# Performance work log

Hardware: AMD Instinct MI355X
Metric: run time of the kernel (lower is better)

The kernel has to match this reference:

```python
import jax, jax.numpy as jnp
import numpy as np

D = 1024          # d_model
DQ = D // 4       # embedding dim (d_model//4)
DH = D // 2       # head hidden (d_model//2)
P = 6             # n_digit_positions = max_int_digits + n_decimal_digits
NOPS, NPT = 9, 10
B, T = 8, 2048


def _ln(x, g, b, eps=1e-5):
    m = jnp.mean(x, axis=-1, keepdims=True)
    v = jnp.mean(jnp.square(x - m), axis=-1, keepdims=True)
    return (x - m) * jax.lax.rsqrt(v + eps) * g + b


def _xavier(key, shape):
    fan_in, fan_out = shape[-2], shape[-1]
    lim = np.sqrt(6.0 / (fan_in + fan_out))
    return jax.random.uniform(key, shape, jnp.float32, -lim, lim)


def setup_inputs() -> dict:
    key = jax.random.key(0)
    ks = jax.random.split(key, 20)
    inp = {
        'hidden': jax.random.normal(ks[0], (B, T, D), jnp.float32),
        'operation_type': jax.random.randint(ks[1], (B,), 0, NOPS),
        'param_type': jax.random.randint(ks[2], (B, T), 0, NPT),
        # embeddings (std=0.02 like the torch init)
        'op_embed': 0.02 * jax.random.normal(ks[3], (NOPS, DQ), jnp.float32),
        'pt_embed': 0.02 * jax.random.normal(ks[4], (NPT, DQ), jnp.float32),
        'pos_embed': 0.02 * jax.random.normal(ks[5], (P, DQ), jnp.float32),
        # context_proj: Linear(D + D//2 -> D) + LayerNorm(D)
        'ctx_w': _xavier(ks[6], (D + D // 2, D)),
        'ctx_b': jnp.zeros((D,), jnp.float32),
        'ctx_g': jnp.ones((D,), jnp.float32),
        'ctx_beta': jnp.zeros((D,), jnp.float32),
        # sign_head: Linear(D->DH), LN(DH), Linear(DH->3)
        'sign_w1': _xavier(ks[7], (D, DH)),
        'sign_b1': jnp.zeros((DH,), jnp.float32),
        'sign_g': jnp.ones((DH,), jnp.float32),
        'sign_beta': jnp.zeros((DH,), jnp.float32),
        'sign_w2': _xavier(ks[8], (DH, 3)),
        'sign_b2': jnp.zeros((3,), jnp.float32),
        # digit heads stacked over positions: Linear(D+DQ->DH), LN(DH), Linear(DH->10)
        'dig_w1': _xavier(ks[9], (P, D + DQ, DH)),
        'dig_b1': jnp.zeros((P, DH), jnp.float32),
        'dig_g': jnp.ones((P, DH), jnp.float32),
        'dig_beta': jnp.zeros((P, DH), jnp.float32),
        'dig_w2': _xavier(ks[10], (P, DH, 10)),
        'dig_b2': jnp.zeros((P, 10), jnp.float32),
        'aux_w1': _xavier(ks[11], (D, DH)),
        'aux_b1': jnp.zeros((DH,), jnp.float32),
        'aux_w2': _xavier(ks[12], (DH, 1)),
        'aux_b2': jnp.zeros((1,), jnp.float32),
    }
    return inp


def reference(hidden, operation_type, param_type, op_embed, pt_embed, pos_embed,
              ctx_w, ctx_b, ctx_g, ctx_beta,
              sign_w1, sign_b1, sign_g, sign_beta, sign_w2, sign_b2,
              dig_w1, dig_b1, dig_g, dig_beta, dig_w2, dig_b2,
              aux_w1, aux_b1, aux_w2, aux_b2):
    b, t, d = hidden.shape
    gelu = lambda x: jax.nn.gelu(x, approximate=False)  # torch nn.GELU default

    op_emb = jnp.broadcast_to(op_embed[operation_type][:, None, :], (b, t, DQ))
    pm_emb = pt_embed[param_type]                       # [B,T,DQ]
    ctx_in = jnp.concatenate([hidden, op_emb, pm_emb], axis=-1)  # [B,T,1.5D]
    context = gelu(_ln(ctx_in @ ctx_w + ctx_b, ctx_g, ctx_beta))  # [B,T,D]

    sh = gelu(_ln(context @ sign_w1 + sign_b1, sign_g, sign_beta))
    sign_logits = sh @ sign_w2 + sign_b2                # [B,T,3]

    # digit heads, vectorized over position. concat(context, pos_emb[p]) @ W1
    # == context @ W1[:, :D] + pos_emb[p] @ W1[:, D:]
    h = (jnp.einsum('btd,pdh->btph', context, dig_w1[:, :D, :])
         + jnp.einsum('pq,pqh->ph', pos_embed, dig_w1[:, D:, :])
         + dig_b1)                                      # [B,T,P,DH]
    h = gelu(_ln(h, dig_g, dig_beta))
    digit_logits = jnp.einsum('btph,pho->btpo', h, dig_w2) + dig_b2  # [B,T,P,10]

    aux_value = gelu(context @ aux_w1 + aux_b1) @ aux_w2 + aux_b2    # [B,T,1]

    return sign_logits, digit_logits, aux_value
```

## Files before the change

### kernel.cpp

```cpp
#include <hip/hip_runtime.h>
#include <hip/hip_bf16.h>

typedef unsigned short u16;
typedef __attribute__((ext_vector_type(8))) __bf16 bf16x8;
typedef __attribute__((ext_vector_type(4))) float f32x4;

typedef __attribute__((address_space(1))) const void GVoid;
typedef __attribute__((address_space(3))) void LVoid;

__device__ __forceinline__ void async_load16(const u16* g, u16* l) {
    __builtin_amdgcn_global_load_lds((GVoid*)g, (LVoid*)l, 16, 0, 0);
}

__device__ __forceinline__ float bf2f(u16 u) {
    union { unsigned i; float f; } v; v.i = ((unsigned)u) << 16; return v.f;
}
__device__ __forceinline__ u16 f2bf(float f) {
    union { float f; unsigned i; } v; v.f = f;
    unsigned r = (v.i + 0x7FFFu + ((v.i >> 16) & 1u)) >> 16;
    return (u16)r;
}
__device__ __forceinline__ float gelu_f(float x) {
    float t = x * fmaf(0.0356774081f, x * x, 0.7978845608f);
    float e = __expf(2.0f * t);
    float r = 1.0f / (e + 1.0f);
    return x - x * r;
}

#define OP_E   0
#define PT_E   2304
#define POS_E  4864
#define CTX_B  6400
#define CTX_G  7424
#define CTX_BE 8448
#define S_B1   9472
#define S_G    9984
#define S_BE   10496
#define S_B2   11008
#define D_G    11012
#define D_BE   14084
#define D_B2   17156
#define A_B1   17216
#define A_B2   17728

struct SmallTab {
    const float* src[15];
    int off[15];
    int cnt[15];
};

__global__ __launch_bounds__(256) void convert_small(SmallTab tab, u16* __restrict__ dst)
{
    int idx = blockIdx.x * 256 + threadIdx.x;
#pragma unroll
    for (int e = 0; e < 15; ++e) {
        if (idx < tab.cnt[e]) {
            dst[tab.off[e] + idx] = f2bf(tab.src[e][idx]);
            return;
        }
        idx -= tab.cnt[e];
    }
}

__global__ __launch_bounds__(256) void transpose_all(
    const float* __restrict__ ctx_w, const float* __restrict__ sign_w1,
    const float* __restrict__ aux_w1, const float* __restrict__ dig_w1,
    u16* __restrict__ ctxWt, u16* __restrict__ BtAll)
{
    __shared__ u16 tl[32][33];
    int z = blockIdx.z;
    const float* src; u16* dst; size_t srcOff = 0; int srcLd, cols;
    if (z == 8) { src = ctx_w; dst = ctxWt; srcLd = 1024; cols = 1024; }
    else {
        srcLd = 512; cols = 512;
        if (z == 0) src = sign_w1;
        else if (z == 1) src = aux_w1;
        else { src = dig_w1; srcOff = (size_t)(z - 2) * 1280 * 512; }
        dst = BtAll + (size_t)z * 512 * 1024;
    }
    int n0 = blockIdx.x * 32;
    if (n0 >= cols) return;
    int k0 = blockIdx.y * 32;
    int t = threadIdx.x;
    int r = t >> 3;
    int c4 = (t & 7) * 4;
    float4 v = *(const float4*)&src[srcOff + (size_t)(k0 + r) * srcLd + n0 + c4];
    tl[r][c4 + 0] = f2bf(v.x); tl[r][c4 + 1] = f2bf(v.y);
    tl[r][c4 + 2] = f2bf(v.z); tl[r][c4 + 3] = f2bf(v.w);
    __syncthreads();
    ushort4 o;
    o.x = tl[c4 + 0][r]; o.y = tl[c4 + 1][r]; o.z = tl[c4 + 2][r]; o.w = tl[c4 + 3][r];
    *(ushort4*)&dst[(size_t)(n0 + r) * 1024 + k0 + c4] = o;
}

__global__ __launch_bounds__(256) void precompute_bias(
    const float* __restrict__ ctx_w, const float* __restrict__ dig_w1,
    const float* __restrict__ op_embed, const float* __restrict__ pt_embed,
    const float* __restrict__ pos_embed, const float* __restrict__ dig_b1,
    const int* __restrict__ op_type,
    float* __restrict__ E_op, float* __restrict__ P_pt, float* __restrict__ dbias)
{
    int idx = blockIdx.x * 256 + threadIdx.x;
    if (idx < 8192) {
        int b = idx >> 10, n = idx & 1023;
        const float* e = op_embed + op_type[b] * 256;
        float s = 0.f;
        for (int q = 0; q < 256; ++q)
            s += e[q] * ctx_w[(size_t)(1024 + q) * 1024 + n];
        E_op[idx] = s;
    } else if (idx < 18432) {
        int i = idx - 8192;
        int v = i >> 10, n = i & 1023;
        const float* e = pt_embed + v * 256;
        float s = 0.f;
        for (int q = 0; q < 256; ++q)
            s += e[q] * ctx_w[(size_t)(1280 + q) * 1024 + n];
        P_pt[i] = s;
    } else if (idx < 21504) {
        int i = idx - 18432;
        int p = i >> 9, h = i & 511;
        const float* e = pos_embed + p * 256;
        float s = dig_b1[p * 512 + h];
        for (int q = 0; q < 256; ++q)
            s += e[q] * dig_w1[(size_t)p * 1280 * 512 + (size_t)(1024 + q) * 512 + h];
        dbias[i] = s;
    }
}

__global__ __launch_bounds__(256) void build_vec(
    const u16* __restrict__ csm, const float* __restrict__ dbias,
    float* __restrict__ biasAll, float* __restrict__ gammaAll,
    float* __restrict__ betaAll)
{
    int n = blockIdx.x * 256 + threadIdx.x;
    float bi, g, be;
    if (n < 512) {
        bi = bf2f(csm[S_B1 + n]); g = bf2f(csm[S_G + n]); be = bf2f(csm[S_BE + n]);
    } else if (n < 1024) {
        bi = bf2f(csm[A_B1 + n - 512]); g = 1.f; be = 0.f;
    } else {
        int h = n - 1024;
        bi = dbias[h]; g = bf2f(csm[D_G + h]); be = bf2f(csm[D_BE + h]);
    }
    biasAll[n] = bi; gammaAll[n] = g; betaAll[n] = be;
}

__global__ __launch_bounds__(256) void build_w2pad(
    const float* __restrict__ sign_w2, const float* __restrict__ dig_w2,
    const float* __restrict__ aux_w2, u16* __restrict__ W2pad)
{
    int idx = blockIdx.x * 256 + threadIdx.x;
    int row = idx >> 12, k = idx & 4095;
    int r = row >> 4, o = row & 15;
    float v = 0.f;
    if (r == 0) {
        if (o < 3 && k < 512) v = sign_w2[k * 3 + o];
    } else if (r == 7) {
        if (o == 0 && k >= 512 && k < 1024) v = aux_w2[k - 512];
    } else {
        int p = r - 1, lo = 1024 + p * 512;
        if (o < 10 && k >= lo && k < lo + 512) v = dig_w2[(size_t)p * 5120 + (k - lo) * 10 + o];
    }
    W2pad[idx] = f2bf(v);
}

__global__ __launch_bounds__(512) void gemm_head_8ph(
    const u16* __restrict__ A, const u16* __restrict__ Bt, u16* __restrict__ C,
    int M)
{
    __shared__ u16 smem[65536];
    const int tid = threadIdx.x;
    const int wid = tid >> 6, lane = tid & 63;
    const int quad = lane >> 4, r16 = lane & 15;
    const int wm = wid >> 2, wn = wid & 3;

    const int Mtiles = M >> 8;
    int flat = blockIdx.x + blockIdx.y * gridDim.x;
    int cpx = (Mtiles * 16) >> 3;
    int swz = (flat & 7) * cpx + (flat >> 3);
    int bm = swz % Mtiles, bn = swz / Mtiles;
    const int m0 = bm << 8, n0 = bn << 8;

    const int rb = tid >> 3;
    const int cx = ((tid & 7) ^ (rb & 7)) * 8;
    const u16* gA = A + (size_t)(m0 + rb) * 1024 + cx;
    const u16* gB = Bt + (size_t)(n0 + rb) * 1024 + cx;

#define STAGE(arr, h, tt) do { \
        u16* _d = smem + ((((tt) & 1) * 2 + (arr)) * 2 + (h)) * 8192 + wid * 512; \
        const u16* _s = ((arr) ? gB : gA) + (size_t)((h) * 128) * 1024 + (tt) * 64; \
        async_load16(_s, _d); \
        async_load16(_s + (size_t)64 * 1024, _d + 4096); \
    } while (0)

    STAGE(0, 0, 0); STAGE(0, 1, 0); STAGE(1, 0, 0); STAGE(1, 1, 0);
    STAGE(0, 0, 1); STAGE(0, 1, 1); STAGE(1, 0, 1);
    asm volatile("s_waitcnt vmcnt(6)" ::: "memory");
    asm volatile("s_barrier" ::: "memory");

    f32x4 acc[8][4] = {};
    const int kx0 = ((quad) ^ (r16 & 7)) * 8;
    const int kx1 = ((4 + quad) ^ (r16 & 7)) * 8;

#define QUAD(MF0, NF0) \
        _Pragma("unroll") \
        for (int ks = 0; ks < 2; ++ks) \
            _Pragma("unroll") \
            for (int mi = 0; mi < 4; ++mi) \
                _Pragma("unroll") \
                for (int nj = 0; nj < 2; ++nj) \
                    acc[(MF0) + mi][(NF0) + nj] = \
                        __builtin_amdgcn_mfma_f32_16x16x32_bf16( \
                            afr[(MF0) + mi][ks], bfr[(NF0) + nj][ks], \
                            acc[(MF0) + mi][(NF0) + nj], 0, 0, 0);

    for (int t = 0; t < 16; ++t) {
        const int cur = t & 1;
        const u16* sA = smem + cur * 32768 + wm * 8192 + r16 * 64;
        const u16* sB = smem + cur * 32768 + 16384 + (wn >> 1) * 8192
                        + ((wn & 1) * 64 + r16) * 64;

        if (t + 1 < 16) STAGE(1, 1, t + 1);
        bf16x8 afr[8][2], bfr[4][2];
#pragma unroll
        for (int mf = 0; mf < 8; ++mf) {
            afr[mf][0] = *(const bf16x8*)&sA[mf * 1024 + kx0];
            afr[mf][1] = *(const bf16x8*)&sA[mf * 1024 + kx1];
        }
#pragma unroll
        for (int nf = 0; nf < 4; ++nf) {
            bfr[nf][0] = *(const bf16x8*)&sB[nf * 1024 + kx0];
            bfr[nf][1] = *(const bf16x8*)&sB[nf * 1024 + kx1];
        }
        __builtin_amdgcn_s_setprio(1);
        QUAD(0, 0)
        __builtin_amdgcn_s_setprio(0);
        asm volatile("s_waitcnt lgkmcnt(0)" ::: "memory");
        __builtin_amdgcn_sched_barrier(0);
        asm volatile("s_barrier" ::: "memory");
        __builtin_amdgcn_sched_barrier(0);

        if (t + 2 < 16) STAGE(0, 0, t + 2);
        __builtin_amdgcn_sched_barrier(0);
        __builtin_amdgcn_s_setprio(1);
        QUAD(0, 2)
        __builtin_amdgcn_s_setprio(0);
        __builtin_amdgcn_sched_barrier(0);
        asm volatile("s_barrier" ::: "memory");
        __builtin_amdgcn_sched_barrier(0);

        if (t + 2 < 16) STAGE(0, 1, t + 2);
        __builtin_amdgcn_sched_barrier(0);
        __builtin_amdgcn_s_setprio(1);
        QUAD(4, 0)
        __builtin_amdgcn_s_setprio(0);
        __builtin_amdgcn_sched_barrier(0);
        asm volatile("s_barrier" ::: "memory");
        __builtin_amdgcn_sched_barrier(0);

        if (t + 2 < 16) STAGE(1, 0, t + 2);
        __builtin_amdgcn_sched_barrier(0);
        __builtin_amdgcn_s_setprio(1);
        QUAD(4, 2)
        __builtin_amdgcn_s_setprio(0);
        __builtin_amdgcn_sched_barrier(0);
        if (t < 14)       asm volatile("s_waitcnt vmcnt(6)" ::: "memory");
        else if (t == 14) asm volatile("s_waitcnt vmcnt(0)" ::: "memory");
        asm volatile("s_barrier" ::: "memory");
    }
#undef QUAD
#undef STAGE

#pragma unroll
    for (int mf = 0; mf < 8; ++mf) {
#pragma unroll
        for (int nf = 0; nf < 4; ++nf) {
            size_t base = (size_t)(m0 + wm * 128 + mf * 16 + quad * 4) * 4096
                          + n0 + wn * 64 + nf * 16 + r16;
#pragma unroll
            for (int r = 0; r < 4; ++r)
                C[base + (size_t)r * 4096] = f2bf(acc[mf][nf][r]);
        }
    }
}

__global__ __launch_bounds__(256) void gemm_f32a(
    const float* __restrict__ A, const u16* __restrict__ Bt, u16* __restrict__ C,
    int M, int N, int K)
{
    __shared__ u16 As[128 * 32];
    __shared__ u16 Bs[128 * 32];
    const int tid = threadIdx.x;
    const int wid = tid >> 6, lane = tid & 63;
    const int m0 = blockIdx.x * 128, n0 = blockIdx.y * 128;
    const int mw = (wid >> 1) * 64, nw = (wid & 1) * 64;
    const int quad = lane >> 4, r16 = lane & 15;

    f32x4 acc[4][4] = {};

    const int srow = wid * 32 + (lane >> 2);
    const int scol = (lane & 3) * 8;
    const u16* gB = Bt + (size_t)(n0 + srow) * K + scol;
    u16* lB = Bs + wid * 32 * 32;

    const int r0 = tid >> 2;
    const int c8 = (tid & 3) * 8;

    for (int k0 = 0; k0 < K; k0 += 32) {
        async_load16(gB + k0, lB);
        async_load16(gB + k0 + (size_t)16 * K, lB + 16 * 32);
        const float* p0 = &A[(size_t)(m0 + r0) * K + k0 + c8];
        const float* p1 = &A[(size_t)(m0 + 64 + r0) * K + k0 + c8];
        float4 x = *(const float4*)p0, y = *(const float4*)(p0 + 4);
        float4 u = *(const float4*)p1, w = *(const float4*)(p1 + 4);
        uint4 a0, a1;
        a0.x = f2bf(x.x) | ((unsigned)f2bf(x.y) << 16);
        a0.y = f2bf(x.z) | ((unsigned)f2bf(x.w) << 16);
        a0.z = f2bf(y.x) | ((unsigned)f2bf(y.y) << 16);
        a0.w = f2bf(y.z) | ((unsigned)f2bf(y.w) << 16);
        a1.x = f2bf(u.x) | ((unsigned)f2bf(u.y) << 16);
        a1.y = f2bf(u.z) | ((unsigned)f2bf(u.w) << 16);
        a1.z = f2bf(w.x) | ((unsigned)f2bf(w.y) << 16);
        a1.w = f2bf(w.z) | ((unsigned)f2bf(w.w) << 16);
        *(uint4*)&As[r0 * 32 + c8] = a0;
        *(uint4*)&As[(64 + r0) * 32 + c8] = a1;
        __syncthreads();

        bf16x8 af[4], bw[4];
#pragma unroll
        for (int i = 0; i < 4; ++i)
            af[i] = *(const bf16x8*)&As[(mw + i * 16 + r16) * 32 + quad * 8];
#pragma unroll
        for (int j = 0; j < 4; ++j)
            bw[j] = *(const bf16x8*)&Bs[(nw + j * 16 + r16) * 32 + quad * 8];
#pragma unroll
        for (int i = 0; i < 4; ++i)
#pragma unroll
            for (int j = 0; j < 4; ++j)
                acc[i][j] = __builtin_amdgcn_mfma_f32_16x16x32_bf16(
                    af[i], bw[j], acc[i][j], 0, 0, 0);
        __syncthreads();
    }

#pragma unroll
    for (int i = 0; i < 4; ++i) {
#pragma unroll
        for (int j = 0; j < 4; ++j) {
            int col = n0 + nw + j * 16 + r16;
            size_t base = (size_t)(m0 + mw + i * 16 + quad * 4) * N + col;
#pragma unroll
            for (int r = 0; r < 4; ++r)
                C[base + (size_t)r * N] = f2bf(acc[i][j][r]);
        }
    }
}

__global__ __launch_bounds__(256) void ln_ctx_kernel(
    const u16* __restrict__ pre, const float* __restrict__ E_op,
    const float* __restrict__ P_pt, const int* __restrict__ ptype,
    const u16* __restrict__ csm, u16* __restrict__ ctx, int tokOff)
{
    __shared__ float red[8];
    int local = blockIdx.x;
    int token = tokOff + local;
    int b = token >> 11;
    int pt = ptype[token];
    int tid = threadIdx.x;
    int c = tid * 4;
    int wid = tid >> 6, lane = tid & 63;

    ushort4 xp = *(const ushort4*)&pre[(size_t)local * 1024 + c];
    float4 eo = *(const float4*)&E_op[b * 1024 + c];
    float4 pp = *(const float4*)&P_pt[pt * 1024 + c];
    ushort4 cb4 = *(const ushort4*)&csm[CTX_B + c];
    float x[4];
    x[0] = bf2f(xp.x) + eo.x + pp.x + bf2f(cb4.x);
    x[1] = bf2f(xp.y) + eo.y + pp.y + bf2f(cb4.y);
    x[2] = bf2f(xp.z) + eo.z + pp.z + bf2f(cb4.z);
    x[3] = bf2f(xp.w) + eo.w + pp.w + bf2f(cb4.w);

    float s = x[0] + x[1] + x[2] + x[3];
    float s2 = x[0]*x[0] + x[1]*x[1] + x[2]*x[2] + x[3]*x[3];
    for (int off = 32; off; off >>= 1) { s += __shfl_xor(s, off); s2 += __shfl_xor(s2, off); }
    if (lane == 0) { red[wid] = s; red[4 + wid] = s2; }
    __syncthreads();
    s  = red[0] + red[1] + red[2] + red[3];
    s2 = red[4] + red[5] + red[6] + red[7];
    float mean = s * (1.f / 1024.f);
    float var = fmaxf(s2 * (1.f / 1024.f) - mean * mean, 0.f);
    float rs = rsqrtf(var + 1e-5f);

    ushort4 g4 = *(const ushort4*)&csm[CTX_G + c];
    ushort4 b4 = *(const ushort4*)&csm[CTX_BE + c];
    ushort4 o;
    o.x = f2bf(gelu_f((x[0] - mean) * rs * bf2f(g4.x) + bf2f(b4.x)));
    o.y = f2bf(gelu_f((x[1] - mean) * rs * bf2f(g4.y) + bf2f(b4.y)));
    o.z = f2bf(gelu_f((x[2] - mean) * rs * bf2f(g4.z) + bf2f(b4.z)));
    o.w = f2bf(gelu_f((x[3] - mean) * rs * bf2f(g4.w) + bf2f(b4.w)));
    *(ushort4*)&ctx[(size_t)token * 1024 + c] = o;
}

__global__ __launch_bounds__(256) void ln_stats(
    const u16* __restrict__ hp, const float* __restrict__ biasAll,
    float2* __restrict__ stats, int Rh)
{
    int wid = threadIdx.x >> 6, lane = threadIdx.x & 63;
    int idx = blockIdx.x * 4 + wid;
    int token = idx >> 3, s = idx & 7;
    const u16* row = hp + (size_t)token * 4096 + s * 512 + lane * 8;
    ushort4 a = ((const ushort4*)row)[0];
    ushort4 b = ((const ushort4*)row)[1];
    u16 xr[8]; *(ushort4*)&xr[0] = a; *(ushort4*)&xr[4] = b;
    const float* bi = biasAll + s * 512 + lane * 8;
    float4 b0 = *(const float4*)bi, b1 = *(const float4*)(bi + 4);
    float bb[8] = {b0.x, b0.y, b0.z, b0.w, b1.x, b1.y, b1.z, b1.w};
    float sm = 0.f, s2 = 0.f;
#pragma unroll
    for (int j = 0; j < 8; ++j) {
        float v = bf2f(xr[j]) + bb[j];
        sm += v; s2 += v * v;
    }
    for (int off = 32; off; off >>= 1) { sm += __shfl_xor(sm, off); s2 += __shfl_xor(s2, off); }
    if (lane == 0) {
        float mean = sm * (1.f / 512.f);
        float var = fmaxf(s2 * (1.f / 512.f) - mean * mean, 0.f);
        float2 st = make_float2(mean, rsqrtf(var + 1e-5f));
        if (s == 1) st = make_float2(0.f, 1.f);
        stats[idx] = st;
    }
}

__global__ __launch_bounds__(256) void gemm_final(
    const u16* __restrict__ A, const u16* __restrict__ W2pad,
    const float* __restrict__ biasAll, const float* __restrict__ gammaAll,
    const float* __restrict__ betaAll, const float2* __restrict__ stats,
    float* __restrict__ out_pre, int Rh)
{
    __shared__ u16 As[128 * 32];
    __shared__ u16 Bs[128 * 32];
    const int tid = threadIdx.x;
    const int wid = tid >> 6, lane = tid & 63;
    const int m0 = blockIdx.x * 128;
    const int ks = blockIdx.y, kbase = ks * 1024;
    const int mw = (wid >> 1) * 64, nw = (wid & 1) * 64;
    const int quad = lane >> 4, r16 = lane & 15;

    f32x4 acc[4][4] = {};

    const int srow = wid * 32 + (lane >> 2);
    const int scol = (lane & 3) * 8;
    const u16* gB = W2pad + (size_t)srow * 4096 + kbase + scol;
    u16* lB = Bs + wid * 32 * 32;

    const int r0 = tid >> 2;
    const int c8 = (tid & 3) * 8;

    for (int k0 = 0; k0 < 1024; k0 += 32) {
        async_load16(gB + k0, lB);
        async_load16(gB + k0 + (size_t)16 * 4096, lB + 16 * 32);
        int kk = kbase + k0 + c8;
        int sl = kk >> 9;
        float4 bi0 = *(const float4*)&biasAll[kk], bi1 = *(const float4*)&biasAll[kk + 4];
        float4 g0 = *(const float4*)&gammaAll[kk], g1 = *(const float4*)&gammaAll[kk + 4];
        float4 be0 = *(const float4*)&betaAll[kk], be1 = *(const float4*)&betaAll[kk + 4];
        float bb[8] = {bi0.x, bi0.y, bi0.z, bi0.w, bi1.x, bi1.y, bi1.z, bi1.w};
        float gg[8] = {g0.x, g0.y, g0.z, g0.w, g1.x, g1.y, g1.z, g1.w};
        float bt[8] = {be0.x, be0.y, be0.z, be0.w, be1.x, be1.y, be1.z, be1.w};
#pragma unroll
        for (int h = 0; h < 2; ++h) {
            int row = m0 + r0 + h * 64;
            const u16* ap = A + (size_t)row * 4096 + kk;
            ushort4 xa = ((const ushort4*)ap)[0];
            ushort4 xb = ((const ushort4*)ap)[1];
            u16 xr[8]; *(ushort4*)&xr[0] = xa; *(ushort4*)&xr[4] = xb;
            float2 st = stats[row * 8 + sl];
            u16 o[8];
#pragma unroll
            for (int j = 0; j < 8; ++j) {
                float v = (bf2f(xr[j]) + bb[j] - st.x) * st.y * gg[j] + bt[j];
                o[j] = f2bf(gelu_f(v));
            }
            *(uint4*)&As[(h * 64 + r0) * 32 + c8] = *(const uint4*)&o[0];
        }
        __syncthreads();

        bf16x8 af[4], bw[4];
#pragma unroll
        for (int i = 0; i < 4; ++i)
            af[i] = *(const bf16x8*)&As[(mw + i * 16 + r16) * 32 + quad * 8];
#pragma unroll
        for (int j = 0; j < 4; ++j)
            bw[j] = *(const bf16x8*)&Bs[(nw + j * 16 + r16) * 32 + quad * 8];
#pragma unroll
        for (int i = 0; i < 4; ++i)
#pragma unroll
            for (int j = 0; j < 4; ++j)
                acc[i][j] = __builtin_amdgcn_mfma_f32_16x16x32_bf16(
                    af[i], bw[j], acc[i][j], 0, 0, 0);
        __syncthreads();
    }

    float* op = out_pre + (size_t)ks * Rh * 128;
#pragma unroll
    for (int i = 0; i < 4; ++i) {
#pragma unroll
        for (int j = 0; j < 4; ++j) {
            int col = nw + j * 16 + r16;
            size_t base = (size_t)(m0 + mw + i * 16 + quad * 4) * 128 + col;
#pragma unroll
            for (int r = 0; r < 4; ++r)
                op[base + (size_t)r * 128] = acc[i][j][r];
        }
    }
}

__global__ __launch_bounds__(256) void gather_out(
    const float* __restrict__ out_pre, const u16* __restrict__ csm,
    float* __restrict__ out, int tokOff, int Rh)
{
    int idx = blockIdx.x * 256 + threadIdx.x;
    if (idx >= Rh * 64) return;
    int local = idx >> 6;
    int c = idx & 63;
    int token = tokOff + local;
    size_t P = (size_t)Rh * 128;
    size_t base = (size_t)local * 128;
    int col;
    if (c < 3) col = c;
    else if (c == 63) col = 7 * 16;
    else { int d = c - 3; int p = d / 10; col = (p + 1) * 16 + (d - p * 10); }
    float v = out_pre[base + col] + out_pre[P + base + col]
            + out_pre[2 * P + base + col] + out_pre[3 * P + base + col];
    if (c < 3) {
        out[(size_t)token * 3 + c] = v + bf2f(csm[S_B2 + c]);
    } else if (c == 63) {
        out[1032192 + (size_t)token] = v + bf2f(csm[A_B2]);
    } else {
        int d = c - 3;
        int p = d / 10, o = d - p * 10;
        out[49152 + ((size_t)token * 6 + p) * 10 + o] = v + bf2f(csm[D_B2 + p * 10 + o]);
    }
}

extern "C" void kernel_launch(void* const* d_in, const int* in_sizes, int n_in,
                              void* d_out, int out_size, void* d_ws, size_t ws_size,
                              hipStream_t stream) {
    const float* hidden    = (const float*)d_in[0];
    const int*   op_type   = (const int*)d_in[1];
    const int*   pt_type   = (const int*)d_in[2];
    const float* op_embed  = (const float*)d_in[3];
    const float* pt_embed  = (const float*)d_in[4];
    const float* pos_embed = (const float*)d_in[5];
    const float* ctx_w     = (const float*)d_in[6];
    const float* sign_w1   = (const float*)d_in[10];
    const float* sign_w2   = (const float*)d_in[14];
    const float* dig_w1    = (const float*)d_in[16];
    const float* dig_b1    = (const float*)d_in[17];
    const float* dig_w2    = (const float*)d_in[20];
    const float* aux_w1    = (const float*)d_in[22];
    const float* aux_w2    = (const float*)d_in[24];

    char* ws = (char*)d_ws;
    u16*    ctxWt    = (u16*)(ws + 0);
    u16*    BtAll    = (u16*)(ws + 2097152);
    float*  E_op     = (float*)(ws + 10485760);
    float*  P_pt     = (float*)(ws + 10518528);
    float*  dbias    = (float*)(ws + 10559488);
    u16*    csm      = (u16*)(ws + 10571776);
    float*  biasAll  = (float*)(ws + 10637312);
    float*  gammaAll = (float*)(ws + 10653696);
    float*  betaAll  = (float*)(ws + 10670080);
    float2* stats    = (float2*)(ws + 10686464);
    u16*    context  = (u16*)(ws + 11735040);
    u16*    scratch  = (u16*)(ws + 45289472);
    u16*    W2pad    = ctxWt;
    size_t S = (ws_size > 45289472) ? ws_size - 45289472 : 0;

    int Rc = 16384;
    while ((size_t)Rc * 2048 > S && Rc > 128) Rc >>= 1;
    int Rh = 16384;
    while ((size_t)Rh * 8192 > S && Rh > 256) Rh >>= 1;

    float* out = (float*)d_out;

    SmallTab tab;
    const float* srcs[15] = { op_embed, pt_embed, pos_embed,
                              (const float*)d_in[7], (const float*)d_in[8], (const float*)d_in[9],
                              (const float*)d_in[11], (const float*)d_in[12], (const float*)d_in[13],
                              (const float*)d_in[15],
                              (const float*)d_in[18], (const float*)d_in[19], (const float*)d_in[21],
                              (const float*)d_in[23], (const float*)d_in[25] };
    const int offs[15] = { OP_E, PT_E, POS_E, CTX_B, CTX_G, CTX_BE,
                           S_B1, S_G, S_BE, S_B2,
                           D_G, D_BE, D_B2, A_B1, A_B2 };
    const int cnts[15] = { 2304, 2560, 1536, 1024, 1024, 1024,
                           512, 512, 512, 3,
                           3072, 3072, 60, 512, 1 };
    for (int i = 0; i < 15; ++i) { tab.src[i] = srcs[i]; tab.off[i] = offs[i]; tab.cnt[i] = cnts[i]; }
    convert_small<<<70, 256, 0, stream>>>(tab, csm);

    transpose_all<<<dim3(32, 32, 9), 256, 0, stream>>>(
        ctx_w, sign_w1, aux_w1, dig_w1, ctxWt, BtAll);
    precompute_bias<<<84, 256, 0, stream>>>(
        ctx_w, dig_w1, op_embed, pt_embed, pos_embed, dig_b1, op_type,
        E_op, P_pt, dbias);
    build_vec<<<16, 256, 0, stream>>>(csm, dbias, biasAll, gammaAll, betaAll);

    for (int t0 = 0; t0 < 16384; t0 += Rc) {
        gemm_f32a<<<dim3(Rc / 128, 8), 256, 0, stream>>>(
            hidden + (size_t)t0 * 1024, ctxWt, scratch, Rc, 1024, 1024);
        ln_ctx_kernel<<<Rc, 256, 0, stream>>>(
            scratch, E_op, P_pt, pt_type, csm, context, t0);
    }

    build_w2pad<<<2048, 256, 0, stream>>>(sign_w2, dig_w2, aux_w2, W2pad);

    for (int t0 = 0; t0 < 16384; t0 += Rh) {
        gemm_head_8ph<<<dim3(Rh / 256, 16), 512, 0, stream>>>(
            context + (size_t)t0 * 1024, BtAll, scratch, Rh);
        ln_stats<<<Rh * 2, 256, 0, stream>>>(scratch, biasAll, stats, Rh);
        float* out_pre = (float*)(context + (size_t)t0 * 1024);
        gemm_final<<<dim3(Rh / 128, 4), 256, 0, stream>>>(
            scratch, W2pad, biasAll, gammaAll, betaAll, stats, out_pre, Rh);
        gather_out<<<(Rh * 64 + 255) / 256, 256, 0, stream>>>(
            out_pre, csm, out, t0, Rh);
    }
}
```

Before: 522.3 us.

## Reuse pipelined 8-phase GEMM for context projection and fuse LN stats into head GEMM

The fp32-input context GEMM is replaced by a separate pass that converts hidden to bf16, followed by the templated 256x256 8-phase pipelined GEMM that the heads already use. The head GEMM epilogue now computes per-row partial sums and sums of squares and accumulates them with atomics, replacing the separate ln_stats kernel that re-read the large intermediate. Small zero and finalize kernels are added. The cost is an extra full pass over hidden plus atomic traffic, and the order of the floating-point reductions is no longer deterministic.

```diff
diff --git a/kernel.cpp b/kernel.cpp
--- a/kernel.cpp
+++ b/kernel.cpp
@@ -60,6 +60,21 @@
         }
         idx -= tab.cnt[e];
     }
+}
+
+__global__ __launch_bounds__(256) void convert_hidden(
+    const float* __restrict__ src, u16* __restrict__ dst, int n8)
+{
+    int i = blockIdx.x * 256 + threadIdx.x;
+    if (i >= n8) return;
+    const float4* p = (const float4*)(src + (size_t)i * 8);
+    float4 a = p[0], b = p[1];
+    uint4 o;
+    o.x = f2bf(a.x) | ((unsigned)f2bf(a.y) << 16);
+    o.y = f2bf(a.z) | ((unsigned)f2bf(a.w) << 16);
+    o.z = f2bf(b.x) | ((unsigned)f2bf(b.y) << 16);
+    o.w = f2bf(b.z) | ((unsigned)f2bf(b.w) << 16);
+    *(uint4*)(dst + (size_t)i * 8) = o;
 }
 
 __global__ __launch_bounds__(256) void transpose_all(
@@ -164,9 +179,29 @@
     W2pad[idx] = f2bf(v);
 }
 
-__global__ __launch_bounds__(512) void gemm_head_8ph(
+__global__ __launch_bounds__(256) void zero_stats(float2* __restrict__ stats, int n)
+{
+    int i = blockIdx.x * 256 + threadIdx.x;
+    if (i < n) stats[i] = make_float2(0.f, 0.f);
+}
+
+__global__ __launch_bounds__(256) void stats_fin(float2* __restrict__ stats, int Rh)
+{
+    int i = blockIdx.x * 256 + threadIdx.x;
+    if (i >= Rh * 8) return;
+    int s = i & 7;
+    float2 v = stats[i];
+    float mean = v.x * (1.f / 512.f);
+    float var = fmaxf(v.y * (1.f / 512.f) - mean * mean, 0.f);
+    float2 o = make_float2(mean, rsqrtf(var + 1e-5f));
+    if (s == 1) o = make_float2(0.f, 1.f);
+    stats[i] = o;
+}
+
+template<bool STATS>
+__global__ __launch_bounds__(512) void gemm_8ph(
     const u16* __restrict__ A, const u16* __restrict__ Bt, u16* __restrict__ C,
-    int M)
+    int M, int N, const float* __restrict__ biasAll, float* __restrict__ statSums)
 {
     __shared__ u16 smem[65536];
     const int tid = threadIdx.x;
@@ -176,7 +211,7 @@
 
     const int Mtiles = M >> 8;
     int flat = blockIdx.x + blockIdx.y * gridDim.x;
-    int cpx = (Mtiles * 16) >> 3;
+    int cpx = (Mtiles * (N >> 8)) >> 3;
     int swz = (flat & 7) * cpx + (flat >> 3);
     int bm = swz % Mtiles, bn = swz / Mtiles;
     const int m0 = bm << 8, n0 = bn << 8;
@@ -271,86 +306,44 @@
 #undef QUAD
 #undef STAGE
 
+    if constexpr (STATS) {
+        float bnf[4];
+#pragma unroll
+        for (int nf = 0; nf < 4; ++nf)
+            bnf[nf] = biasAll[n0 + wn * 64 + nf * 16 + r16];
+        const int sl = n0 >> 9;
+#pragma unroll
+        for (int mf = 0; mf < 8; ++mf) {
+#pragma unroll
+            for (int r = 0; r < 4; ++r) {
+                float sv = 0.f, s2v = 0.f;
+#pragma unroll
+                for (int nf = 0; nf < 4; ++nf) {
+                    float v = bf2f(f2bf(acc[mf][nf][r])) + bnf[nf];
+                    sv += v; s2v += v * v;
+                }
+                sv += __shfl_xor(sv, 8);  s2v += __shfl_xor(s2v, 8);
+                sv += __shfl_xor(sv, 4);  s2v += __shfl_xor(s2v, 4);
+                sv += __shfl_xor(sv, 2);  s2v += __shfl_xor(s2v, 2);
+                sv += __shfl_xor(sv, 1);  s2v += __shfl_xor(s2v, 1);
+                if (r16 == 0) {
+                    int row = m0 + wm * 128 + mf * 16 + quad * 4 + r;
+                    atomicAdd(&statSums[((size_t)row * 8 + sl) * 2], sv);
+                    atomicAdd(&statSums[((size_t)row * 8 + sl) * 2 + 1], s2v);
+                }
+            }
+        }
+    }
+
 #pragma unroll
     for (int mf = 0; mf < 8; ++mf) {
 #pragma unroll
         for (int nf = 0; nf < 4; ++nf) {
-            size_t base = (size_t)(m0 + wm * 128 + mf * 16 + quad * 4) * 4096
+            size_t base = (size_t)(m0 + wm * 128 + mf * 16 + quad * 4) * N
                           + n0 + wn * 64 + nf * 16 + r16;
 #pragma unroll
             for (int r = 0; r < 4; ++r)
-                C[base + (size_t)r * 4096] = f2bf(acc[mf][nf][r]);
-        }
-    }
-}
-
-__global__ __launch_bounds__(256) void gemm_f32a(
-    const float* __restrict__ A, const u16* __restrict__ Bt, u16* __restrict__ C,
-    int M, int N, int K)
-{
-    __shared__ u16 As[128 * 32];
-    __shared__ u16 Bs[128 * 32];
-    const int tid = threadIdx.x;
-    const int wid = tid >> 6, lane = tid & 63;
-    const int m0 = blockIdx.x * 128, n0 = blockIdx.y * 128;
-    const int mw = (wid >> 1) * 64, nw = (wid & 1) * 64;
-    const int quad = lane >> 4, r16 = lane & 15;
-
-    f32x4 acc[4][4] = {};
-
-    const int srow = wid * 32 + (lane >> 2);
-    const int scol = (lane & 3) * 8;
-    const u16* gB = Bt + (size_t)(n0 + srow) * K + scol;
-    u16* lB = Bs + wid * 32 * 32;
-
-    const int r0 = tid >> 2;
-    const int c8 = (tid & 3) * 8;
-
-    for (int k0 = 0; k0 < K; k0 += 32) {
-        async_load16(gB + k0, lB);
-        async_load16(gB + k0 + (size_t)16 * K, lB + 16 * 32);
-        const float* p0 = &A[(size_t)(m0 + r0) * K + k0 + c8];
-        const float* p1 = &A[(size_t)(m0 + 64 + r0) * K + k0 + c8];
-        float4 x = *(const float4*)p0, y = *(const float4*)(p0 + 4);
-        float4 u = *(const float4*)p1, w = *(const float4*)(p1 + 4);
-        uint4 a0, a1;
-        a0.x = f2bf(x.x) | ((unsigned)f2bf(x.y) << 16);
-        a0.y = f2bf(x.z) | ((unsigned)f2bf(x.w) << 16);
-        a0.z = f2bf(y.x) | ((unsigned)f2bf(y.y) << 16);
-        a0.w = f2bf(y.z) | ((unsigned)f2bf(y.w) << 16);
-        a1.x = f2bf(u.x) | ((unsigned)f2bf(u.y) << 16);
-        a1.y = f2bf(u.z) | ((unsigned)f2bf(u.w) << 16);
-        a1.z = f2bf(w.x) | ((unsigned)f2bf(w.y) << 16);
-        a1.w = f2bf(w.z) | ((unsigned)f2bf(w.w) << 16);
-        *(uint4*)&As[r0 * 32 + c8] = a0;
-        *(uint4*)&As[(64 + r0) * 32 + c8] = a1;
-        __syncthreads();
-
-        bf16x8 af[4], bw[4];
-#pragma unroll
-        for (int i = 0; i < 4; ++i)
-            af[i] = *(const bf16x8*)&As[(mw + i * 16 + r16) * 32 + quad * 8];
-#pragma unroll
-        for (int j = 0; j < 4; ++j)
-            bw[j] = *(const bf16x8*)&Bs[(nw + j * 16 + r16) * 32 + quad * 8];
-#pragma unroll
-        for (int i = 0; i < 4; ++i)
-#pragma unroll
-            for (int j = 0; j < 4; ++j)
-                acc[i][j] = __builtin_amdgcn_mfma_f32_16x16x32_bf16(
-                    af[i], bw[j], acc[i][j], 0, 0, 0);
-        __syncthreads();
-    }
-
-#pragma unroll
-    for (int i = 0; i < 4; ++i) {
-#pragma unroll
-        for (int j = 0; j < 4; ++j) {
-            int col = n0 + nw + j * 16 + r16;
-            size_t base = (size_t)(m0 + mw + i * 16 + quad * 4) * N + col;
-#pragma unroll
-            for (int r = 0; r < 4; ++r)
-                C[base + (size_t)r * N] = f2bf(acc[i][j][r]);
+                C[base + (size_t)r * N] = f2bf(acc[mf][nf][r]);
         }
     }
 }
@@ -398,36 +391,6 @@
     o.z = f2bf(gelu_f((x[2] - mean) * rs * bf2f(g4.z) + bf2f(b4.z)));
     o.w = f2bf(gelu_f((x[3] - mean) * rs * bf2f(g4.w) + bf2f(b4.w)));
     *(ushort4*)&ctx[(size_t)token * 1024 + c] = o;
-}
-
-__global__ __launch_bounds__(256) void ln_stats(
-    const u16* __restrict__ hp, const float* __restrict__ biasAll,
-    float2* __restrict__ stats, int Rh)
-{
-    int wid = threadIdx.x >> 6, lane = threadIdx.x & 63;
-    int idx = blockIdx.x * 4 + wid;
-    int token = idx >> 3, s = idx & 7;
-    const u16* row = hp + (size_t)token * 4096 + s * 512 + lane * 8;
-    ushort4 a = ((const ushort4*)row)[0];
-    ushort4 b = ((const ushort4*)row)[1];
-    u16 xr[8]; *(ushort4*)&xr[0] = a; *(ushort4*)&xr[4] = b;
-    const float* bi = biasAll + s * 512 + lane * 8;
-    float4 b0 = *(const float4*)bi, b1 = *(const float4*)(bi + 4);
-    float bb[8] = {b0.x, b0.y, b0.z, b0.w, b1.x, b1.y, b1.z, b1.w};
-    float sm = 0.f, s2 = 0.f;
-#pragma unroll
-    for (int j = 0; j < 8; ++j) {
-        float v = bf2f(xr[j]) + bb[j];
-        sm += v; s2 += v * v;
-    }
-    for (int off = 32; off; off >>= 1) { sm += __shfl_xor(sm, off); s2 += __shfl_xor(s2, off); }
-    if (lane == 0) {
-        float mean = sm * (1.f / 512.f);
-        float var = fmaxf(s2 * (1.f / 512.f) - mean * mean, 0.f);
-        float2 st = make_float2(mean, rsqrtf(var + 1e-5f));
-        if (s == 1) st = make_float2(0.f, 1.f);
-        stats[idx] = st;
-    }
 }
 
 __global__ __launch_bounds__(256) void gemm_final(
@@ -577,7 +540,7 @@
     size_t S = (ws_size > 45289472) ? ws_size - 45289472 : 0;
 
     int Rc = 16384;
-    while ((size_t)Rc * 2048 > S && Rc > 128) Rc >>= 1;
+    while ((size_t)Rc * 2048 > S && Rc > 512) Rc >>= 1;
     int Rh = 16384;
     while ((size_t)Rh * 8192 > S && Rh > 256) Rh >>= 1;
 
@@ -606,9 +569,12 @@
         E_op, P_pt, dbias);
     build_vec<<<16, 256, 0, stream>>>(csm, dbias, biasAll, gammaAll, betaAll);
 
+    u16* hbf16 = context;
+    convert_hidden<<<8192, 256, 0, stream>>>(hidden, hbf16, 16384 * 1024 / 8);
+
     for (int t0 = 0; t0 < 16384; t0 += Rc) {
-        gemm_f32a<<<dim3(Rc / 128, 8), 256, 0, stream>>>(
-            hidden + (size_t)t0 * 1024, ctxWt, scratch, Rc, 1024, 1024);
+        gemm_8ph<false><<<dim3(Rc / 256, 4), 512, 0, stream>>>(
+            hbf16 + (size_t)t0 * 1024, ctxWt, scratch, Rc, 1024, nullptr, nullptr);
         ln_ctx_kernel<<<Rc, 256, 0, stream>>>(
             scratch, E_op, P_pt, pt_type, csm, context, t0);
     }
@@ -616,9 +582,11 @@
     build_w2pad<<<2048, 256, 0, stream>>>(sign_w2, dig_w2, aux_w2, W2pad);
 
     for (int t0 = 0; t0 < 16384; t0 += Rh) {
-        gemm_head_8ph<<<dim3(Rh / 256, 16), 512, 0, stream>>>(
-            context + (size_t)t0 * 1024, BtAll, scratch, Rh);
-        ln_stats<<<Rh * 2, 256, 0, stream>>>(scratch, biasAll, stats, Rh);
+        zero_stats<<<(Rh * 8 + 255) / 256, 256, 0, stream>>>(stats, Rh * 8);
+        gemm_8ph<true><<<dim3(Rh / 256, 16), 512, 0, stream>>>(
+            context + (size_t)t0 * 1024, BtAll, scratch, Rh, 4096,
+            biasAll, (float*)stats);
+        stats_fin<<<(Rh * 8 + 255) / 256, 256, 0, stream>>>(stats, Rh);
         float* out_pre = (float*)(context + (size_t)t0 * 1024);
         gemm_final<<<dim3(Rh / 128, 4), 256, 0, stream>>>(
             scratch, W2pad, biasAll, gammaAll, betaAll, stats, out_pre, Rh);
```

Measured after the change: 580.7 us. 1.11x slower.
